# Kernel tuning notes

Hardware: AMD Instinct MI355X
Metric: run time of the kernel (lower is better)

## Reference

```python
import jax, jax.numpy as jnp
import numpy as np

B, N, DIM = 2, 2048, 1024
HEADS, DIM_HEAD = 8, 64
INNER = HEADS * DIM_HEAD  # 512
EPS = 1e-5  # fp32 branch of the source LayerNorm


def setup_inputs() -> dict:
    key = jax.random.key(0)
    ks = jax.random.split(key, 5)
    x = jax.random.normal(ks[0], (B, N, DIM), dtype=jnp.float32)
    g = jnp.ones((DIM,), dtype=jnp.float32)  # LayerNorm gain init
    # Linear weights stored as (in, out) so y = x @ W. Source zero-inits
    # to_out; we use small random values so the baseline output is nonzero.
    wq = jax.random.normal(ks[1], (DIM, INNER), dtype=jnp.float32) * 0.02
    wkv = jax.random.normal(ks[2], (DIM, 2 * INNER), dtype=jnp.float32) * 0.02
    wo = jax.random.normal(ks[3], (INNER, DIM), dtype=jnp.float32) * 0.02
    return {"x": x, "g": g, "wq": wq, "wkv": wkv, "wo": wo}


def reference(x, g, wq, wkv, wo):
    # Custom LayerNorm from the source: statistics over dim=1 (sequence axis!)
    mean = jnp.mean(x, axis=1, keepdims=True)
    var = jnp.var(x, axis=1, keepdims=True)  # unbiased=False
    xn = (x - mean) * jax.lax.rsqrt(var + EPS) * g  # g broadcasts on last dim

    q = xn @ wq                      # [b, n, inner]
    kv = xn @ wkv                    # [b, n, 2*inner]
    k, v = jnp.split(kv, 2, axis=-1)

    def split_heads(t):  # b n (h d) -> b h n d
        b, n, _ = t.shape
        return t.reshape(b, n, HEADS, DIM_HEAD).transpose(0, 2, 1, 3)

    q, k, v = map(split_heads, (q, k, v))
    q = q * (DIM_HEAD ** -0.5)

    sim = jnp.einsum('bhid,bhjd->bhij', q, k)   # [b, h, n, n]
    attn = jax.nn.softmax(sim, axis=-1)
    out = jnp.einsum('bhij,bhjd->bhid', attn, v)  # [b, h, n, d]

    out = out.transpose(0, 2, 1, 3).reshape(B, N, INNER)  # b h n d -> b n (h d)
    return out @ wo  # [b, n, dim]
```

## Files before the change

kernel.cpp:

```cpp
#include <hip/hip_runtime.h>
#include <hip/hip_bf16.h>
#include <stdint.h>


#define B_ 2
#define N_ 2048
#define DIM_ 1024
#define DH_ 64
#define INNER_ 512
#define ROWS_ 4096
#define QKVN_ 1536
#define POSTRIDE 2097152

#define QSCALE 0.18033688011112042f

typedef __bf16 bf16x8 __attribute__((ext_vector_type(8)));
typedef float floatx4 __attribute__((ext_vector_type(4)));

#if __has_builtin(__builtin_amdgcn_exp2f)
#define EXP2(x) __builtin_amdgcn_exp2f(x)
#else
#define EXP2(x) exp2f(x)
#endif

__device__ __forceinline__ ushort f2bf(float f) {
    union { float f; uint32_t u; } v; v.f = f;
    uint32_t u = v.u;
    u += 0x7fffu + ((u >> 16) & 1u);
    return (ushort)(u >> 16);
}
__device__ __forceinline__ uint32_t pkbf(float a, float b) {
    return (uint32_t)f2bf(a) | ((uint32_t)f2bf(b) << 16);
}
__device__ __forceinline__ void gld_lds(const ushort* g, ushort* l) {
    __builtin_amdgcn_global_load_lds(
        (const __attribute__((address_space(1))) void*)g,
        (__attribute__((address_space(3))) void*)l, 16, 0, 0);
}

__global__ __launch_bounds__(256) void setup_fused(
    const float* __restrict__ x, float* __restrict__ ps, float* __restrict__ pq,
    const float* __restrict__ wq, const float* __restrict__ wkv,
    const float* __restrict__ wo, ushort* __restrict__ wqkv_t,
    ushort* __restrict__ wo_t) {
    __shared__ float tile[32][33];
    int bid = blockIdx.x;
    if (bid < 256) {
        int gd = (bid & 7) * 256 + threadIdx.x;
        int ch = bid >> 3;
        int b = gd >> 10;
        const float* p = x + (size_t)(b * N_ + ch * 64) * DIM_ + (gd & 1023);
        float s = 0.f, q = 0.f;
#pragma unroll 4
        for (int n = 0; n < 64; ++n) { float v = p[(size_t)n * DIM_]; s += v; q += v * v; }
        ps[ch * 2048 + gd] = s;
        pq[ch * 2048 + gd] = q;
        return;
    }
    int t = bid - 256;
    const float* src; ushort* dst; int C; int bx, by; float scale;
    if (t < 512)       { src = wq;  dst = wqkv_t;              C = 512;  scale = QSCALE; bx = t & 31; by = t >> 5; }
    else if (t < 1536) { int u = t - 512;  src = wkv; dst = wqkv_t + 512 * 1024; C = 1024; scale = 1.f; bx = u & 31; by = u >> 5; }
    else               { int u = t - 1536; src = wo;  dst = wo_t;       C = 1024; scale = 1.f; bx = u & 15; by = u >> 4; }
    const int R = (t >= 1536) ? 512 : 1024;
    int r0 = bx * 32, c0 = by * 32;
    int i = threadIdx.x >> 5, j = threadIdx.x & 31;
#pragma unroll
    for (int p = 0; p < 4; ++p)
        tile[i + 8 * p][j] = src[(size_t)(r0 + i + 8 * p) * C + c0 + j] * scale;
    __syncthreads();
#pragma unroll
    for (int p = 0; p < 4; ++p)
        dst[(size_t)(c0 + i + 8 * p) * R + r0 + j] = f2bf(tile[j][i + 8 * p]);
}

__global__ __launch_bounds__(256) void stats_final(
    const float* __restrict__ ps, const float* __restrict__ pq,
    float* __restrict__ meanb, float* __restrict__ rstdb) {
    int gd = blockIdx.x * 256 + threadIdx.x;
    float s = 0.f, q = 0.f;
#pragma unroll
    for (int ch = 0; ch < 32; ++ch) { s += ps[ch * 2048 + gd]; q += pq[ch * 2048 + gd]; }
    float mean = s * (1.f / N_);
    float var = q * (1.f / N_) - mean * mean;
    meanb[gd] = mean;
    rstdb[gd] = rsqrtf(var + 1e-5f);
}

__global__ __launch_bounds__(256) void norm_cast(
    const float* __restrict__ x, const float* __restrict__ g,
    const float* __restrict__ meanb, const float* __restrict__ rstdb,
    ushort* __restrict__ xn) {
    size_t e = ((size_t)blockIdx.x * 256 + threadIdx.x) * 4;
    int c = (int)(e & 1023);
    int b = (int)(e >> 21);
    float4 xv = *(const float4*)&x[e];
    float4 gv = *(const float4*)&g[c];
    float4 mv = *(const float4*)&meanb[b * DIM_ + c];
    float4 rv = *(const float4*)&rstdb[b * DIM_ + c];
    ushort4 o;
    o.x = f2bf((xv.x - mv.x) * rv.x * gv.x);
    o.y = f2bf((xv.y - mv.y) * rv.y * gv.y);
    o.z = f2bf((xv.z - mv.z) * rv.z * gv.z);
    o.w = f2bf((xv.w - mv.w) * rv.w * gv.w);
    *(ushort4*)&xn[e] = o;
}

template <int NI, bool OUT_BF16>
__global__ __launch_bounds__(256) void gemm_bt(
    const ushort* __restrict__ A, const ushort* __restrict__ Bt,
    void* __restrict__ C, int M, int N, int K) {
    constexpr int TN = 32 * NI;
    __shared__ __align__(16) ushort sA[64 * 64];
    __shared__ __align__(16) ushort sB[TN * 64];
    const int tx = threadIdx.x;
    const int w = tx >> 6, l = tx & 63;
    const int wm = w & 1, wn = w >> 1;
    const int lr = l & 15, lq = l >> 4;
    const int tileM = blockIdx.x * 64;
    const int tileN = blockIdx.y * TN;
    const int rl = l >> 3;
    const int swz8 = ((l & 7) ^ rl) * 8;
    const int fo0 = (lq ^ (lr & 7)) * 8;
    const int fo1 = ((4 + lq) ^ (lr & 7)) * 8;

    floatx4 acc[2][NI] = {};

    for (int k0 = 0; k0 < K; k0 += 64) {
#pragma unroll
        for (int i = 0; i < 2; ++i) {
            int r0 = 16 * w + 8 * i;
            gld_lds(A + (size_t)(tileM + r0 + rl) * K + k0 + swz8, &sA[r0 * 64]);
        }
#pragma unroll
        for (int i = 0; i < TN / 32; ++i) {
            int r0 = (TN / 4) * w + 8 * i;
            gld_lds(Bt + (size_t)(tileN + r0 + rl) * K + k0 + swz8, &sB[r0 * 64]);
        }
        __syncthreads();
#pragma unroll
        for (int s = 0; s < 2; ++s) {
            const int fo = s ? fo1 : fo0;
            bf16x8 a[2], b[NI];
#pragma unroll
            for (int mi = 0; mi < 2; ++mi)
                a[mi] = *(const bf16x8*)&sA[(32 * wm + 16 * mi + lr) * 64 + fo];
#pragma unroll
            for (int ni = 0; ni < NI; ++ni)
                b[ni] = *(const bf16x8*)&sB[(16 * NI * wn + 16 * ni + lr) * 64 + fo];
#pragma unroll
            for (int mi = 0; mi < 2; ++mi)
#pragma unroll
                for (int ni = 0; ni < NI; ++ni)
                    acc[mi][ni] = __builtin_amdgcn_mfma_f32_16x16x32_bf16(
                        a[mi], b[ni], acc[mi][ni], 0, 0, 0);
        }
        __syncthreads();
    }

#pragma unroll
    for (int mi = 0; mi < 2; ++mi)
#pragma unroll
        for (int ni = 0; ni < NI; ++ni)
#pragma unroll
            for (int reg = 0; reg < 4; ++reg) {
                int row = tileM + 32 * wm + 16 * mi + 4 * lq + reg;
                int col = tileN + 16 * NI * wn + 16 * ni + lr;
                float v = acc[mi][ni][reg];
                if (OUT_BF16)
                    ((ushort*)C)[(size_t)row * N + col] = f2bf(v);
                else
                    ((float*)C)[(size_t)row * N + col] = v;
            }
}

__global__ __launch_bounds__(256) void vtrans(
    const ushort* __restrict__ qkv, ushort* __restrict__ vT) {
    __shared__ __align__(16) ushort sT[64 * 72];
    int nt = blockIdx.x, bh = blockIdx.y;
    int b = bh >> 3, h = bh & 7;
    int tx = threadIdx.x;
#pragma unroll
    for (int p = 0; p < 2; ++p) {
        int idx = p * 256 + tx;
        int r = idx >> 3, ch = idx & 7;
        const ushort* gp = qkv + (size_t)(b * N_ + nt * 64 + r) * QKVN_ + 2 * INNER_ + h * DH_ + ch * 8;
        *(uint4*)&sT[r * 72 + ch * 8] = *(const uint4*)gp;
    }
    __syncthreads();
#pragma unroll
    for (int p = 0; p < 2; ++p) {
        int idx = p * 256 + tx;
        int d = idx >> 3, c8 = (idx & 7) * 8;
        union { ushort us[8]; uint4 v; } t;
#pragma unroll
        for (int i = 0; i < 8; ++i) t.us[i] = sT[(c8 + i) * 72 + d];
        *(uint4*)&vT[((size_t)bh * DH_ + d) * N_ + nt * 64 + c8] = t.v;
    }
}

__global__ __launch_bounds__(256, 4) void flash_attn(
    const ushort* __restrict__ qkv, const ushort* __restrict__ vT,
    float* __restrict__ po, float* __restrict__ pl, int nkt) {
    __shared__ __align__(16) ushort sK[64 * 64];
    __shared__ __align__(16) ushort sV[64 * 64];
    __shared__ __align__(16) ushort sPQ[4 * 32 * 72];

    const int tx = threadIdx.x;
    const int w = tx >> 6, l = tx & 63;
    const int lr = l & 15, lq = l >> 4;
    const int qt = blockIdx.x, bh = blockIdx.y, sp = blockIdx.z;
    const int b = bh >> 3, h = bh & 7;
    const size_t rowbase = (size_t)b * N_;
    const int qbase = qt * 128;
    const int kbase = sp * nkt * 64;

    const int rl = l >> 3;
    const int swz8 = ((l & 7) ^ rl) * 8;
    const int fr0 = (lq ^ (lr & 7)) * 8;
    const int fr1 = ((4 + lq) ^ (lr & 7)) * 8;

#pragma unroll
    for (int i = 0; i < 4; ++i) {
        int r0 = 32 * w + 8 * i;
        gld_lds(qkv + (rowbase + qbase + r0 + rl) * QKVN_ + h * DH_ + swz8,
                &sPQ[r0 * 64]);
    }
    __syncthreads();
    bf16x8 bq[2][2];
#pragma unroll
    for (int qq = 0; qq < 2; ++qq) {
        int r = (32 * w + 16 * qq + lr) * 64;
        bq[qq][0] = *(const bf16x8*)&sPQ[r + fr0];
        bq[qq][1] = *(const bf16x8*)&sPQ[r + fr1];
    }

    floatx4 o[2][4] = {};
    float lsum[2] = {0.f, 0.f};

    for (int kt = 0; kt < nkt; ++kt) {
        __syncthreads();
#pragma unroll
        for (int i = 0; i < 2; ++i) {
            int r0 = 16 * w + 8 * i;
            gld_lds(qkv + (rowbase + kbase + kt * 64 + r0 + rl) * QKVN_ + INNER_ + h * DH_ + swz8,
                    &sK[r0 * 64]);
            gld_lds(vT + ((size_t)bh * DH_ + r0 + rl) * N_ + kbase + kt * 64 + swz8,
                    &sV[r0 * 64]);
        }
        __syncthreads();

        floatx4 c[4][2] = {};
#pragma unroll
        for (int s = 0; s < 2; ++s) {
            const int fo = s ? fr1 : fr0;
            bf16x8 ak[4];
#pragma unroll
            for (int kk = 0; kk < 4; ++kk)
                ak[kk] = *(const bf16x8*)&sK[(16 * kk + lr) * 64 + fo];
#pragma unroll
            for (int kk = 0; kk < 4; ++kk)
#pragma unroll
                for (int qq = 0; qq < 2; ++qq)
                    c[kk][qq] = __builtin_amdgcn_mfma_f32_16x16x32_bf16(
                        ak[kk], bq[qq][s], c[kk][qq], 0, 0, 0);
        }

#pragma unroll
        for (int kk = 0; kk < 4; ++kk)
#pragma unroll
            for (int qq = 0; qq < 2; ++qq) {
                float e0 = EXP2(c[kk][qq][0]);
                float e1 = EXP2(c[kk][qq][1]);
                float e2 = EXP2(c[kk][qq][2]);
                float e3 = EXP2(c[kk][qq][3]);
                lsum[qq] += (e0 + e1) + (e2 + e3);
                uint2 u; u.x = pkbf(e0, e1); u.y = pkbf(e2, e3);
                *(uint2*)&sPQ[(32 * w + 16 * qq + lr) * 72 + 16 * kk + 4 * lq] = u;
            }

#pragma unroll
        for (int s = 0; s < 2; ++s) {
            const int fo = s ? fr1 : fr0;
            bf16x8 ap[2], bv[4];
#pragma unroll
            for (int mi = 0; mi < 2; ++mi)
                ap[mi] = *(const bf16x8*)&sPQ[(32 * w + 16 * mi + lr) * 72 + 32 * s + 8 * lq];
#pragma unroll
            for (int dt = 0; dt < 4; ++dt)
                bv[dt] = *(const bf16x8*)&sV[(16 * dt + lr) * 64 + fo];
#pragma unroll
            for (int mi = 0; mi < 2; ++mi)
#pragma unroll
                for (int dt = 0; dt < 4; ++dt)
                    o[mi][dt] = __builtin_amdgcn_mfma_f32_16x16x32_bf16(
                        ap[mi], bv[dt], o[mi][dt], 0, 0, 0);
        }
    }

#pragma unroll
    for (int qq = 0; qq < 2; ++qq) {
        lsum[qq] += __shfl_xor(lsum[qq], 16);
        lsum[qq] += __shfl_xor(lsum[qq], 32);
    }
    float* pob = po + (size_t)sp * POSTRIDE;
    if (lq == 0) {
#pragma unroll
        for (int qq = 0; qq < 2; ++qq)
            pl[((size_t)sp * 16 + bh) * N_ + qbase + 32 * w + 16 * qq + lr] = lsum[qq];
    }
    const size_t obase = (size_t)bh * N_;
#pragma unroll
    for (int mi = 0; mi < 2; ++mi)
#pragma unroll
        for (int dt = 0; dt < 4; ++dt)
#pragma unroll
            for (int reg = 0; reg < 4; ++reg) {
                int row = qbase + 32 * w + 16 * mi + 4 * lq + reg;
                pob[(obase + row) * DH_ + 16 * dt + lr] = o[mi][dt][reg];
            }
}

__global__ __launch_bounds__(256) void merge_attn(
    const float* __restrict__ po, const float* __restrict__ pl,
    ushort* __restrict__ attn, int nsplit) {
    int idx = blockIdx.x * 256 + threadIdx.x;
    int d4 = (idx & 15) * 4;
    int h = (idx >> 4) & 7;
    int rowg = idx >> 7;
    int b = rowg >> 11, r = rowg & 2047;
    size_t pbase = ((size_t)b * 8 + h) * N_ + r;
    float4 acc = *(const float4*)&po[pbase * DH_ + d4];
    float lv = pl[pbase];
    for (int s = 1; s < nsplit; ++s) {
        float4 a1 = *(const float4*)&po[(size_t)s * POSTRIDE + pbase * DH_ + d4];
        acc.x += a1.x; acc.y += a1.y; acc.z += a1.z; acc.w += a1.w;
        lv += pl[((size_t)s * 16) * N_ + pbase];
    }
    float inv = 1.f / lv;
    ushort4 ov;
    ov.x = f2bf(acc.x * inv); ov.y = f2bf(acc.y * inv);
    ov.z = f2bf(acc.z * inv); ov.w = f2bf(acc.w * inv);
    *(ushort4*)&attn[(size_t)rowg * INNER_ + h * DH_ + d4] = ov;
}

extern "C" void kernel_launch(void* const* d_in, const int* in_sizes, int n_in,
                              void* d_out, int out_size, void* d_ws, size_t ws_size,
                              hipStream_t stream) {
    const float* x   = (const float*)d_in[0];
    const float* g   = (const float*)d_in[1];
    const float* wq  = (const float*)d_in[2];
    const float* wkv = (const float*)d_in[3];
    const float* wo  = (const float*)d_in[4];
    float* out = (float*)d_out;

    char* ws = (char*)d_ws;
    float*  psum   = (float*)(ws + 0);
    float*  psqr   = (float*)(ws + 262144);
    float*  meanb  = (float*)(ws + 524288);
    float*  rstdb  = (float*)(ws + 532480);
    ushort* xn     = (ushort*)(ws + 540672);
    ushort* wqkv_t = (ushort*)(ws + 8929280);
    ushort* wo_t   = (ushort*)(ws + 12075008);
    ushort* qkvb   = (ushort*)(ws + 13123584);
    ushort* attnb  = (ushort*)(ws + 25706496);
    ushort* vTb    = (ushort*)(ws + 29900800);
    float*  plb    = (float*)(ws + 34095104);
    float*  pob    = (float*)(ws + 34619392);

    const int nsplit = (ws_size >= (size_t)70 * 1024 * 1024) ? 4
                     : (ws_size >= (size_t)52 * 1024 * 1024) ? 2 : 1;

    setup_fused<<<2304, 256, 0, stream>>>(x, psum, psqr, wq, wkv, wo, wqkv_t, wo_t);
    stats_final<<<8, 256, 0, stream>>>(psum, psqr, meanb, rstdb);
    norm_cast<<<4096, 256, 0, stream>>>(x, g, meanb, rstdb, xn);

    gemm_bt<4, true><<<dim3(64, 12), 256, 0, stream>>>(xn, wqkv_t, qkvb, ROWS_, QKVN_, DIM_);
    vtrans<<<dim3(32, 16), 256, 0, stream>>>(qkvb, vTb);
    flash_attn<<<dim3(16, 16, nsplit), 256, 0, stream>>>(qkvb, vTb, pob, plb, 32 / nsplit);
    merge_attn<<<2048, 256, 0, stream>>>(pob, plb, attnb, nsplit);
    gemm_bt<2, false><<<dim3(64, 16), 256, 0, stream>>>(attnb, wo_t, out, ROWS_, DIM_, INNER_);
}
```

Baseline: 161.8 us.

## Pre-pack GEMM operands into MFMA fragment layout and fuse norm and V-transpose

Weights, normalized activations and attention output are now written directly in an MFMA fragment-major layout, so the GEMMs load operands straight from global memory into registers with double buffering and no LDS staging or barriers. The stats finalization and normalize/cast kernels are merged into one, and the V transpose is folded into the QKV GEMM epilogue, which removes two launches and a round trip through memory. The GEMM tiles grow to 64x128 per 128-thread block with 4x4 accumulators per wave, raising register pressure and giving up LDS-based reuse in exchange for simpler, barrier-free loads.

```diff
diff --git a/kernel.cpp b/kernel.cpp
--- a/kernel.cpp
+++ b/kernel.cpp
@@ -9,7 +9,6 @@
 #define DH_ 64
 #define INNER_ 512
 #define ROWS_ 4096
-#define QKVN_ 1536
 #define POSTRIDE 2097152
 
 #define QSCALE 0.18033688011112042f
@@ -37,12 +36,16 @@
         (const __attribute__((address_space(1))) void*)g,
         (__attribute__((address_space(3))) void*)l, 16, 0, 0);
 }
+__device__ __forceinline__ size_t frag_off(int m, int k, int nkc) {
+    return ((size_t)((m >> 4) * nkc + (k >> 5)) * 64 +
+            (size_t)((m & 15) | (((k >> 3) & 3) << 4))) * 8 + (k & 7);
+}
 
 __global__ __launch_bounds__(256) void setup_fused(
     const float* __restrict__ x, float* __restrict__ ps, float* __restrict__ pq,
     const float* __restrict__ wq, const float* __restrict__ wkv,
-    const float* __restrict__ wo, ushort* __restrict__ wqkv_t,
-    ushort* __restrict__ wo_t) {
+    const float* __restrict__ wo, ushort* __restrict__ wqkv_f,
+    ushort* __restrict__ wo_f) {
     __shared__ float tile[32][33];
     int bid = blockIdx.x;
     if (bid < 256) {
@@ -58,149 +61,184 @@
         return;
     }
     int t = bid - 256;
-    const float* src; ushort* dst; int C; int bx, by; float scale;
-    if (t < 512)       { src = wq;  dst = wqkv_t;              C = 512;  scale = QSCALE; bx = t & 31; by = t >> 5; }
-    else if (t < 1536) { int u = t - 512;  src = wkv; dst = wqkv_t + 512 * 1024; C = 1024; scale = 1.f; bx = u & 31; by = u >> 5; }
-    else               { int u = t - 1536; src = wo;  dst = wo_t;       C = 1024; scale = 1.f; bx = u & 15; by = u >> 4; }
-    const int R = (t >= 1536) ? 512 : 1024;
-    int r0 = bx * 32, c0 = by * 32;
-    int i = threadIdx.x >> 5, j = threadIdx.x & 31;
+    const float* src; ushort* dst; int C, K, k0, ncol0, nglob0; float scale;
+    if (t < 512) {
+        int kt = t >> 4, nt = t & 15;
+        src = wq; dst = wqkv_f; C = 512; K = 1024; scale = QSCALE;
+        k0 = kt * 32; ncol0 = nt * 32; nglob0 = ncol0;
+    } else if (t < 1536) {
+        int u = t - 512; int kt = u >> 5, nt = u & 31;
+        src = wkv; dst = wqkv_f; C = 1024; K = 1024; scale = 1.f;
+        k0 = kt * 32; ncol0 = nt * 32; nglob0 = 512 + ncol0;
+    } else {
+        int u = t - 1536; int kt = u >> 5, nt = u & 31;
+        src = wo; dst = wo_f; C = 1024; K = 512; scale = 1.f;
+        k0 = kt * 32; ncol0 = nt * 32; nglob0 = ncol0;
+    }
+    int ti = threadIdx.x >> 5, tj = threadIdx.x & 31;
 #pragma unroll
     for (int p = 0; p < 4; ++p)
-        tile[i + 8 * p][j] = src[(size_t)(r0 + i + 8 * p) * C + c0 + j] * scale;
+        tile[ti + 8 * p][tj] = src[(size_t)(k0 + ti + 8 * p) * C + ncol0 + tj] * scale;
     __syncthreads();
-#pragma unroll
-    for (int p = 0; p < 4; ++p)
-        dst[(size_t)(c0 + i + 8 * p) * R + r0 + j] = f2bf(tile[j][i + 8 * p]);
-}
-
-__global__ __launch_bounds__(256) void stats_final(
+    if (threadIdx.x < 128) {
+        int nl = threadIdx.x & 31, kc8 = threadIdx.x >> 5;
+        union { ushort us[8]; uint4 v; } u;
+#pragma unroll
+        for (int ii = 0; ii < 8; ++ii) u.us[ii] = f2bf(tile[kc8 * 8 + ii][nl]);
+        *(uint4*)&dst[frag_off(nglob0 + nl, k0 + kc8 * 8, K >> 5)] = u.v;
+    }
+}
+
+__global__ __launch_bounds__(256) void finalize_norm(
     const float* __restrict__ ps, const float* __restrict__ pq,
-    float* __restrict__ meanb, float* __restrict__ rstdb) {
-    int gd = blockIdx.x * 256 + threadIdx.x;
-    float s = 0.f, q = 0.f;
-#pragma unroll
-    for (int ch = 0; ch < 32; ++ch) { s += ps[ch * 2048 + gd]; q += pq[ch * 2048 + gd]; }
-    float mean = s * (1.f / N_);
-    float var = q * (1.f / N_) - mean * mean;
-    meanb[gd] = mean;
-    rstdb[gd] = rsqrtf(var + 1e-5f);
-}
-
-__global__ __launch_bounds__(256) void norm_cast(
     const float* __restrict__ x, const float* __restrict__ g,
-    const float* __restrict__ meanb, const float* __restrict__ rstdb,
-    ushort* __restrict__ xn) {
-    size_t e = ((size_t)blockIdx.x * 256 + threadIdx.x) * 4;
-    int c = (int)(e & 1023);
-    int b = (int)(e >> 21);
-    float4 xv = *(const float4*)&x[e];
-    float4 gv = *(const float4*)&g[c];
-    float4 mv = *(const float4*)&meanb[b * DIM_ + c];
-    float4 rv = *(const float4*)&rstdb[b * DIM_ + c];
-    ushort4 o;
-    o.x = f2bf((xv.x - mv.x) * rv.x * gv.x);
-    o.y = f2bf((xv.y - mv.y) * rv.y * gv.y);
-    o.z = f2bf((xv.z - mv.z) * rv.z * gv.z);
-    o.w = f2bf((xv.w - mv.w) * rv.w * gv.w);
-    *(ushort4*)&xn[e] = o;
-}
-
-template <int NI, bool OUT_BF16>
-__global__ __launch_bounds__(256) void gemm_bt(
-    const ushort* __restrict__ A, const ushort* __restrict__ Bt,
-    void* __restrict__ C, int M, int N, int K) {
-    constexpr int TN = 32 * NI;
-    __shared__ __align__(16) ushort sA[64 * 64];
-    __shared__ __align__(16) ushort sB[TN * 64];
-    const int tx = threadIdx.x;
-    const int w = tx >> 6, l = tx & 63;
-    const int wm = w & 1, wn = w >> 1;
-    const int lr = l & 15, lq = l >> 4;
-    const int tileM = blockIdx.x * 64;
-    const int tileN = blockIdx.y * TN;
-    const int rl = l >> 3;
-    const int swz8 = ((l & 7) ^ rl) * 8;
-    const int fo0 = (lq ^ (lr & 7)) * 8;
-    const int fo1 = ((4 + lq) ^ (lr & 7)) * 8;
-
-    floatx4 acc[2][NI] = {};
-
-    for (int k0 = 0; k0 < K; k0 += 64) {
-#pragma unroll
-        for (int i = 0; i < 2; ++i) {
-            int r0 = 16 * w + 8 * i;
-            gld_lds(A + (size_t)(tileM + r0 + rl) * K + k0 + swz8, &sA[r0 * 64]);
-        }
-#pragma unroll
-        for (int i = 0; i < TN / 32; ++i) {
-            int r0 = (TN / 4) * w + 8 * i;
-            gld_lds(Bt + (size_t)(tileN + r0 + rl) * K + k0 + swz8, &sB[r0 * 64]);
-        }
-        __syncthreads();
-#pragma unroll
-        for (int s = 0; s < 2; ++s) {
-            const int fo = s ? fo1 : fo0;
-            bf16x8 a[2], b[NI];
-#pragma unroll
-            for (int mi = 0; mi < 2; ++mi)
-                a[mi] = *(const bf16x8*)&sA[(32 * wm + 16 * mi + lr) * 64 + fo];
-#pragma unroll
-            for (int ni = 0; ni < NI; ++ni)
-                b[ni] = *(const bf16x8*)&sB[(16 * NI * wn + 16 * ni + lr) * 64 + fo];
-#pragma unroll
-            for (int mi = 0; mi < 2; ++mi)
-#pragma unroll
-                for (int ni = 0; ni < NI; ++ni)
-                    acc[mi][ni] = __builtin_amdgcn_mfma_f32_16x16x32_bf16(
-                        a[mi], b[ni], acc[mi][ni], 0, 0, 0);
-        }
-        __syncthreads();
-    }
-
-#pragma unroll
-    for (int mi = 0; mi < 2; ++mi)
-#pragma unroll
-        for (int ni = 0; ni < NI; ++ni)
+    ushort* __restrict__ xnf) {
+    __shared__ float s4[4][64], q4[4][64], aa[64], bb[64];
+    int t = threadIdx.x;
+    int b = blockIdx.x >> 8, slab = (blockIdx.x >> 4) & 15, nch = blockIdx.x & 15;
+    int c0 = slab * 64;
+    {
+        int c = t & 63, grp = t >> 6;
+        float s = 0.f, q = 0.f;
+#pragma unroll
+        for (int ch = 0; ch < 8; ++ch) {
+            int o = (grp * 8 + ch) * 2048 + b * 1024 + c0 + c;
+            s += ps[o]; q += pq[o];
+        }
+        s4[grp][c] = s; q4[grp][c] = q;
+    }
+    __syncthreads();
+    if (t < 64) {
+        float s = s4[0][t] + s4[1][t] + s4[2][t] + s4[3][t];
+        float q = q4[0][t] + q4[1][t] + q4[2][t] + q4[3][t];
+        float mean = s * (1.f / N_);
+        float var = q * (1.f / N_) - mean * mean;
+        float rstd = rsqrtf(var + 1e-5f);
+        float a = rstd * g[c0 + t];
+        aa[t] = a; bb[t] = -mean * a;
+    }
+    __syncthreads();
+    int c4 = (t & 15) * 4, ro = t >> 4;
+#pragma unroll
+    for (int it = 0; it < 8; ++it) {
+        int r = nch * 128 + it * 16 + ro;
+        int m = b * 2048 + r;
+        float4 xv = *(const float4*)&x[(size_t)m * DIM_ + c0 + c4];
+        float v0 = xv.x * aa[c4 + 0] + bb[c4 + 0];
+        float v1 = xv.y * aa[c4 + 1] + bb[c4 + 1];
+        float v2 = xv.z * aa[c4 + 2] + bb[c4 + 2];
+        float v3 = xv.w * aa[c4 + 3] + bb[c4 + 3];
+        uint2 u; u.x = pkbf(v0, v1); u.y = pkbf(v2, v3);
+        *(uint2*)&xnf[frag_off(m, c0 + c4, 32)] = u;
+    }
+}
+
+template <int NKC>
+__device__ __forceinline__ void gemm_core(
+    const ushort* __restrict__ pA, const ushort* __restrict__ pB,
+    floatx4 (&acc)[4][4]) {
+    constexpr int TS = NKC * 512;
+    bf16x8 a0[4], b0[4], a1[4], b1[4];
+#pragma unroll
+    for (int i = 0; i < 4; ++i) {
+        a0[i] = *(const bf16x8*)(pA + (size_t)i * TS);
+        b0[i] = *(const bf16x8*)(pB + (size_t)i * TS);
+    }
+    for (int kc = 0; kc < NKC; kc += 2) {
+#pragma unroll
+        for (int i = 0; i < 4; ++i) {
+            a1[i] = *(const bf16x8*)(pA + (size_t)i * TS + (size_t)(kc + 1) * 512);
+            b1[i] = *(const bf16x8*)(pB + (size_t)i * TS + (size_t)(kc + 1) * 512);
+        }
+#pragma unroll
+        for (int mi = 0; mi < 4; ++mi)
+#pragma unroll
+            for (int ni = 0; ni < 4; ++ni)
+                acc[mi][ni] = __builtin_amdgcn_mfma_f32_16x16x32_bf16(
+                    a0[mi], b0[ni], acc[mi][ni], 0, 0, 0);
+        if (kc + 2 < NKC) {
+#pragma unroll
+            for (int i = 0; i < 4; ++i) {
+                a0[i] = *(const bf16x8*)(pA + (size_t)i * TS + (size_t)(kc + 2) * 512);
+                b0[i] = *(const bf16x8*)(pB + (size_t)i * TS + (size_t)(kc + 2) * 512);
+            }
+        }
+#pragma unroll
+        for (int mi = 0; mi < 4; ++mi)
+#pragma unroll
+            for (int ni = 0; ni < 4; ++ni)
+                acc[mi][ni] = __builtin_amdgcn_mfma_f32_16x16x32_bf16(
+                    a1[mi], b1[ni], acc[mi][ni], 0, 0, 0);
+    }
+}
+
+__global__ __launch_bounds__(128) void gemm_qkv(
+    const ushort* __restrict__ xnf, const ushort* __restrict__ wf,
+    ushort* __restrict__ qk, ushort* __restrict__ vT) {
+    int tx = threadIdx.x, w = tx >> 6, l = tx & 63;
+    int lr = l & 15, lq = l >> 4;
+    int bx = blockIdx.x, by = blockIdx.y;
+    const ushort* pA = xnf + (size_t)(bx * 4) * 32 * 512 + l * 8;
+    const ushort* pB = wf + (size_t)(by * 8 + w * 4) * 32 * 512 + l * 8;
+    floatx4 acc[4][4] = {};
+    gemm_core<32>(pA, pB, acc);
+    int col0 = by * 128 + w * 64;
+    if (by < 8) {
+#pragma unroll
+        for (int mi = 0; mi < 4; ++mi)
+#pragma unroll
+            for (int ni = 0; ni < 4; ++ni) {
+                int col = col0 + 16 * ni + lr;
+#pragma unroll
+                for (int reg = 0; reg < 4; ++reg) {
+                    int row = bx * 64 + 16 * mi + 4 * lq + reg;
+                    qk[(size_t)row * 1024 + col] = f2bf(acc[mi][ni][reg]);
+                }
+            }
+    } else {
+#pragma unroll
+        for (int mi = 0; mi < 4; ++mi) {
+            int row0 = bx * 64 + 16 * mi + 4 * lq;
+            int bb2 = row0 >> 11, nn = row0 & 2047;
+#pragma unroll
+            for (int ni = 0; ni < 4; ++ni) {
+                int cv = col0 - 1024 + 16 * ni + lr;
+                int h = cv >> 6, d = cv & 63;
+                uint2 u;
+                u.x = pkbf(acc[mi][ni][0], acc[mi][ni][1]);
+                u.y = pkbf(acc[mi][ni][2], acc[mi][ni][3]);
+                *(uint2*)&vT[((size_t)((bb2 * 8 + h) * 64 + d)) * 2048 + nn] = u;
+            }
+        }
+    }
+}
+
+__global__ __launch_bounds__(128) void gemm_out(
+    const ushort* __restrict__ af, const ushort* __restrict__ wf,
+    float* __restrict__ out) {
+    int tx = threadIdx.x, w = tx >> 6, l = tx & 63;
+    int lr = l & 15, lq = l >> 4;
+    int bx = blockIdx.x, by = blockIdx.y;
+    const ushort* pA = af + (size_t)(bx * 4) * 16 * 512 + l * 8;
+    const ushort* pB = wf + (size_t)(by * 8 + w * 4) * 16 * 512 + l * 8;
+    floatx4 acc[4][4] = {};
+    gemm_core<16>(pA, pB, acc);
+    int col0 = by * 128 + w * 64;
+#pragma unroll
+    for (int mi = 0; mi < 4; ++mi)
+#pragma unroll
+        for (int ni = 0; ni < 4; ++ni) {
+            int col = col0 + 16 * ni + lr;
 #pragma unroll
             for (int reg = 0; reg < 4; ++reg) {
-                int row = tileM + 32 * wm + 16 * mi + 4 * lq + reg;
-                int col = tileN + 16 * NI * wn + 16 * ni + lr;
-                float v = acc[mi][ni][reg];
-                if (OUT_BF16)
-                    ((ushort*)C)[(size_t)row * N + col] = f2bf(v);
-                else
-                    ((float*)C)[(size_t)row * N + col] = v;
-            }
-}
-
-__global__ __launch_bounds__(256) void vtrans(
-    const ushort* __restrict__ qkv, ushort* __restrict__ vT) {
-    __shared__ __align__(16) ushort sT[64 * 72];
-    int nt = blockIdx.x, bh = blockIdx.y;
-    int b = bh >> 3, h = bh & 7;
-    int tx = threadIdx.x;
-#pragma unroll
-    for (int p = 0; p < 2; ++p) {
-        int idx = p * 256 + tx;
-        int r = idx >> 3, ch = idx & 7;
-        const ushort* gp = qkv + (size_t)(b * N_ + nt * 64 + r) * QKVN_ + 2 * INNER_ + h * DH_ + ch * 8;
-        *(uint4*)&sT[r * 72 + ch * 8] = *(const uint4*)gp;
-    }
-    __syncthreads();
-#pragma unroll
-    for (int p = 0; p < 2; ++p) {
-        int idx = p * 256 + tx;
-        int d = idx >> 3, c8 = (idx & 7) * 8;
-        union { ushort us[8]; uint4 v; } t;
-#pragma unroll
-        for (int i = 0; i < 8; ++i) t.us[i] = sT[(c8 + i) * 72 + d];
-        *(uint4*)&vT[((size_t)bh * DH_ + d) * N_ + nt * 64 + c8] = t.v;
-    }
+                int row = bx * 64 + 16 * mi + 4 * lq + reg;
+                out[(size_t)row * 1024 + col] = acc[mi][ni][reg];
+            }
+        }
 }
 
 __global__ __launch_bounds__(256, 4) void flash_attn(
-    const ushort* __restrict__ qkv, const ushort* __restrict__ vT,
+    const ushort* __restrict__ qk, const ushort* __restrict__ vT,
     float* __restrict__ po, float* __restrict__ pl, int nkt) {
     __shared__ __align__(16) ushort sK[64 * 64];
     __shared__ __align__(16) ushort sV[64 * 64];
@@ -223,7 +261,7 @@
 #pragma unroll
     for (int i = 0; i < 4; ++i) {
         int r0 = 32 * w + 8 * i;
-        gld_lds(qkv + (rowbase + qbase + r0 + rl) * QKVN_ + h * DH_ + swz8,
+        gld_lds(qk + (rowbase + qbase + r0 + rl) * 1024 + h * DH_ + swz8,
                 &sPQ[r0 * 64]);
     }
     __syncthreads();
@@ -243,7 +281,7 @@
 #pragma unroll
         for (int i = 0; i < 2; ++i) {
             int r0 = 16 * w + 8 * i;
-            gld_lds(qkv + (rowbase + kbase + kt * 64 + r0 + rl) * QKVN_ + INNER_ + h * DH_ + swz8,
+            gld_lds(qk + (rowbase + kbase + kt * 64 + r0 + rl) * 1024 + 512 + h * DH_ + swz8,
                     &sK[r0 * 64]);
             gld_lds(vT + ((size_t)bh * DH_ + r0 + rl) * N_ + kbase + kt * 64 + swz8,
                     &sV[r0 * 64]);
@@ -323,7 +361,7 @@
 
 __global__ __launch_bounds__(256) void merge_attn(
     const float* __restrict__ po, const float* __restrict__ pl,
-    ushort* __restrict__ attn, int nsplit) {
+    ushort* __restrict__ attnf, int nsplit) {
     int idx = blockIdx.x * 256 + threadIdx.x;
     int d4 = (idx & 15) * 4;
     int h = (idx >> 4) & 7;
@@ -338,10 +376,10 @@
         lv += pl[((size_t)s * 16) * N_ + pbase];
     }
     float inv = 1.f / lv;
-    ushort4 ov;
-    ov.x = f2bf(acc.x * inv); ov.y = f2bf(acc.y * inv);
-    ov.z = f2bf(acc.z * inv); ov.w = f2bf(acc.w * inv);
-    *(ushort4*)&attn[(size_t)rowg * INNER_ + h * DH_ + d4] = ov;
+    uint2 u;
+    u.x = pkbf(acc.x * inv, acc.y * inv);
+    u.y = pkbf(acc.z * inv, acc.w * inv);
+    *(uint2*)&attnf[frag_off(rowg, h * DH_ + d4, 16)] = u;
 }
 
 extern "C" void kernel_launch(void* const* d_in, const int* in_sizes, int n_in,
@@ -357,27 +395,22 @@
     char* ws = (char*)d_ws;
     float*  psum   = (float*)(ws + 0);
     float*  psqr   = (float*)(ws + 262144);
-    float*  meanb  = (float*)(ws + 524288);
-    float*  rstdb  = (float*)(ws + 532480);
-    ushort* xn     = (ushort*)(ws + 540672);
-    ushort* wqkv_t = (ushort*)(ws + 8929280);
-    ushort* wo_t   = (ushort*)(ws + 12075008);
-    ushort* qkvb   = (ushort*)(ws + 13123584);
-    ushort* attnb  = (ushort*)(ws + 25706496);
-    ushort* vTb    = (ushort*)(ws + 29900800);
-    float*  plb    = (float*)(ws + 34095104);
-    float*  pob    = (float*)(ws + 34619392);
-
-    const int nsplit = (ws_size >= (size_t)70 * 1024 * 1024) ? 4
-                     : (ws_size >= (size_t)52 * 1024 * 1024) ? 2 : 1;
-
-    setup_fused<<<2304, 256, 0, stream>>>(x, psum, psqr, wq, wkv, wo, wqkv_t, wo_t);
-    stats_final<<<8, 256, 0, stream>>>(psum, psqr, meanb, rstdb);
-    norm_cast<<<4096, 256, 0, stream>>>(x, g, meanb, rstdb, xn);
-
-    gemm_bt<4, true><<<dim3(64, 12), 256, 0, stream>>>(xn, wqkv_t, qkvb, ROWS_, QKVN_, DIM_);
-    vtrans<<<dim3(32, 16), 256, 0, stream>>>(qkvb, vTb);
-    flash_attn<<<dim3(16, 16, nsplit), 256, 0, stream>>>(qkvb, vTb, pob, plb, 32 / nsplit);
-    merge_attn<<<2048, 256, 0, stream>>>(pob, plb, attnb, nsplit);
-    gemm_bt<2, false><<<dim3(64, 16), 256, 0, stream>>>(attnb, wo_t, out, ROWS_, DIM_, INNER_);
-}
+    ushort* xnf    = (ushort*)(ws + 524288);
+    ushort* wqkv_f = (ushort*)(ws + 8912896);
+    ushort* wo_f   = (ushort*)(ws + 12058624);
+    ushort* qkb    = (ushort*)(ws + 13107200);
+    ushort* vTb    = (ushort*)(ws + 21495808);
+    ushort* attnf  = (ushort*)(ws + 25690112);
+    float*  plb    = (float*)(ws + 29884416);
+    float*  pob    = (float*)(ws + 30408704);
+
+    const int nsplit = (ws_size >= (size_t)66 * 1024 * 1024) ? 4
+                     : (ws_size >= (size_t)48 * 1024 * 1024) ? 2 : 1;
+
+    setup_fused<<<2304, 256, 0, stream>>>(x, psum, psqr, wq, wkv, wo, wqkv_f, wo_f);
+    finalize_norm<<<512, 256, 0, stream>>>(psum, psqr, x, g, xnf);
+    gemm_qkv<<<dim3(64, 12), 128, 0, stream>>>(xnf, wqkv_f, qkb, vTb);
+    flash_attn<<<dim3(16, 16, nsplit), 256, 0, stream>>>(qkb, vTb, pob, plb, 32 / nsplit);
+    merge_attn<<<2048, 256, 0, stream>>>(pob, plb, attnf, nsplit);
+    gemm_out<<<dim3(64, 8), 128, 0, stream>>>(attnf, wo_f, out);
+}
```

Result: no change. 158.8 us (-1.8%).
